# Performance work log

Hardware: AMD Instinct MI355X
Metric: run time of the kernel (lower is better)

The kernel has to match this reference:

```python
import jax, jax.numpy as jnp
import numpy as np

NUM_FREQS = 6

def posenc(x, num_freqs):
    freqs = (2.0 ** jnp.arange(num_freqs)).astype(x.dtype)  # [F]
    ang = x[..., None] * freqs                               # [N, D, F]
    enc = jnp.concatenate([jnp.sin(ang), jnp.cos(ang)], axis=-1)  # [N, D, 2F]
    return enc.reshape(x.shape[0], -1)

def setup_inputs() -> dict:
    key = jax.random.key(0)
    k1, k2, k3 = jax.random.split(key, 3)
    N, D, C = 200000, 6, 256
    E = D * 2 * NUM_FREQS  # 72
    X = jax.random.normal(k1, (N, D), dtype=jnp.float32)
    linear_mappings = jax.random.normal(k2, (3 * C, E), dtype=jnp.float32) * 0.05
    centroids = jax.random.normal(k3, (C, 3), dtype=jnp.float32)
    return {"X": X, "linear_mappings": linear_mappings, "centroids": centroids}

def reference(X, linear_mappings, centroids):
    N = X.shape[0]
    encoded_X = posenc(X, NUM_FREQS)                         # [N, E]
    rgb_clusters = encoded_X @ linear_mappings.T             # [N, 3C]
    rgb_clusters = rgb_clusters.reshape(N, -1, 3)            # [N, C, 3]
    # scores = centroids @ X[:, :3].T  -> softmax over clusters per point
    scores = X[:, :3] @ centroids.T                          # [N, C] (== scores.T in torch code)
    attention_weights = jax.nn.softmax(scores, axis=-1)      # [N, C]
    # torch does diagonal(attn @ rgb_clusters).T == per-row contraction:
    rgb = jnp.einsum('nc,ncd->nd', attention_weights, rgb_clusters)  # [N, 3]
    return rgb
```

## Files before the change

### kernel.cpp

```cpp
#include <hip/hip_runtime.h>
#include <math.h>


#define NCLUST   256
#define M_BLK    128
#define THREADS  256
#define NTILES   15
#define BG_BYTES (NTILES * 8 * 64 * 16)
#define ENC_STRIDE 168

typedef __attribute__((ext_vector_type(8))) short bfrag_t;
typedef __attribute__((ext_vector_type(4))) float cfrag_t;

static __device__ __forceinline__ unsigned int f2bf_u(float f) {
    unsigned int u = __float_as_uint(f);
    u += 0x7fffu + ((u >> 16) & 1u);
    return u >> 16;
}
static __device__ __forceinline__ unsigned int f2bf2(float lo, float hi) {
    return f2bf_u(lo) | (f2bf_u(hi) << 16);
}
static __device__ __forceinline__ float bf2f(unsigned short s) {
    return __uint_as_float(((unsigned int)s) << 16);
}
static __device__ __forceinline__ void glds16(const void* g, void* l) {
    __builtin_amdgcn_global_load_lds(
        (const __attribute__((address_space(1))) unsigned int*)g,
        (__attribute__((address_space(3))) unsigned int*)l, 16, 0, 0);
}

__global__ void prep_kernel(const float* __restrict__ W, uint4* __restrict__ Bg) {
    const int u = blockIdx.x * 256 + threadIdx.x;
    if (u >= NTILES * 8 * 64) return;
    const int lane = u & 63, ks = (u >> 6) & 7, tile = u >> 9;
    const int ln = lane & 15, q = lane >> 4;
    const int jp = tile * 16 + ln;
    const int d  = jp / 80;
    const int e  = jp - d * 80;
    const int c0 = ks * 32 + q * 8;
    unsigned int w[4] = {0u, 0u, 0u, 0u};
    if (e < 72) {
#pragma unroll
        for (int i = 0; i < 4; ++i) {
            float f0 = W[((c0 + 2 * i)     * 3 + d) * 72 + e];
            float f1 = W[((c0 + 2 * i + 1) * 3 + d) * 72 + e];
            w[i] = f2bf2(f0, f1);
        }
    }
    Bg[u] = make_uint4(w[0], w[1], w[2], w[3]);
}

__global__ __launch_bounds__(THREADS, 2) void rgb_attn_mfma(
    const float* __restrict__ X,
    const float* __restrict__ cent,
    const void* __restrict__ Bg,
    float* __restrict__ out, int N)
{
    __shared__ __align__(16) unsigned char encL[M_BLK * ENC_STRIDE];
    __shared__ __align__(16) unsigned char ABbuf[16384];
    __shared__ float denomL[M_BLK * 2];

    const int tid  = threadIdx.x;
    const int lane = tid & 63;
    const int wv   = tid >> 6;
    const int q    = lane >> 4;
    const int ln   = lane & 15;

    const int pt  = tid & 127;
    const int h   = tid >> 7;
    const int gpt = blockIdx.x * M_BLK + pt;
    const int gp  = (gpt < N) ? gpt : (N - 1);

    float x[6];
#pragma unroll
    for (int k = 0; k < 6; ++k) x[k] = X[gp * 6 + k];

    {
        const int row = tid >> 1, half = tid & 1;
        *(uint2*)(encL + row * ENC_STRIDE + 144 + half * 8) = make_uint2(0u, 0u);
    }
#pragma unroll
    for (int k = 0; k < 3; ++k) {
        const int dd = 3 * h + k;
        const float xv = x[dd];
        float s0,c0,s1,c1,s2,c2,s3,c3,s4,c4,s5,c5;
        __sincosf(xv *  1.0f, &s0, &c0);
        __sincosf(xv *  2.0f, &s1, &c1);
        __sincosf(xv *  4.0f, &s2, &c2);
        __sincosf(xv *  8.0f, &s3, &c3);
        __sincosf(xv * 16.0f, &s4, &c4);
        __sincosf(xv * 32.0f, &s5, &c5);
        unsigned char* rp = encL + pt * ENC_STRIDE + dd * 24;
        *(uint2*)(rp +  0) = make_uint2(f2bf2(s0, s1), f2bf2(s2, s3));
        *(uint2*)(rp +  8) = make_uint2(f2bf2(s4, s5), f2bf2(c0, c1));
        *(uint2*)(rp + 16) = make_uint2(f2bf2(c2, c3), f2bf2(c4, c5));
    }

    bfrag_t afrag[2][8];
    float dpart = 0.0f;
    uint4* AB4 = (uint4*)ABbuf;
#pragma unroll
    for (int p = 0; p < 4; ++p) {
        unsigned int pk[16];
#pragma unroll
        for (int i = 0; i < 16; ++i) {
            const int c0 = p * 64 + h * 32 + 2 * i;
            float sa = fmaf(x[0], cent[c0*3+0], fmaf(x[1], cent[c0*3+1], x[2]*cent[c0*3+2]));
            float sb = fmaf(x[0], cent[c0*3+3], fmaf(x[1], cent[c0*3+4], x[2]*cent[c0*3+5]));
            float ea = __expf(sa), eb_ = __expf(sb);
            dpart += ea + eb_;
            pk[i] = f2bf2(ea, eb_);
        }
        const int bu = ((pt >> 4) * 2 + h) * 64 + (pt & 15);
#pragma unroll
        for (int qq = 0; qq < 4; ++qq)
            AB4[bu + qq * 16] = make_uint4(pk[qq*4+0], pk[qq*4+1], pk[qq*4+2], pk[qq*4+3]);
        if (p == 3) denomL[pt * 2 + h] = dpart;
        __syncthreads();
#pragma unroll
        for (int mt = 0; mt < 2; ++mt)
#pragma unroll
            for (int kw = 0; kw < 2; ++kw)
                afrag[mt][2*p+kw] = *(const bfrag_t*)
                    (ABbuf + (((2*wv+mt)*2 + kw)*64 + lane)*16);
        __syncthreads();
    }

    float part[3][2][4] = {};

#define CONSUME_TILE(T, CT) { \
        cfrag_t a0 = {0.f,0.f,0.f,0.f}, a1 = {0.f,0.f,0.f,0.f}; \
        _Pragma("unroll") \
        for (int ks = 0; ks < 8; ++ks) { \
            const bfrag_t b = *(const bfrag_t*) \
                (ABbuf + (((CT)*8 + ks)*64 + lane)*16); \
            a0 = __builtin_amdgcn_mfma_f32_16x16x32_bf16(afrag[0][ks], b, a0, 0,0,0); \
            a1 = __builtin_amdgcn_mfma_f32_16x16x32_bf16(afrag[1][ks], b, a1, 0,0,0); \
        } \
        const int ebx = ((T) % 5) * 16 + ln; \
        _Pragma("unroll") \
        for (int mt = 0; mt < 2; ++mt) \
        _Pragma("unroll") \
        for (int r = 0; r < 4; ++r) { \
            const int pm = (2*wv + mt)*16 + q*4 + r; \
            const unsigned short us = *(const unsigned short*)(encL + pm*ENC_STRIDE + ebx*2); \
            part[(T)/5][mt][r] = fmaf((mt ? a1[r] : a0[r]), bf2f(us), part[(T)/5][mt][r]); \
        } \
    }

#define STAGE_CHUNK(CC, UNITS) { \
        __syncthreads(); \
        _Pragma("unroll") \
        for (int i = 0; i < 256; i += 64) { \
            if (i < (UNITS) / 4) { \
                const int u = wv * ((UNITS) / 4) + i + lane; \
                glds16((const char*)Bg + ((CC)*1024 + u)*16, (char*)ABbuf + u*16); \
            } } \
        __syncthreads(); \
    }

#define DO_CHUNK_FULL(CC) { \
        STAGE_CHUNK(CC, 1024); \
        CONSUME_TILE(2*(CC), 0); \
        CONSUME_TILE(2*(CC)+1, 1); \
    }

    DO_CHUNK_FULL(0) DO_CHUNK_FULL(1) DO_CHUNK_FULL(2) DO_CHUNK_FULL(3)
    DO_CHUNK_FULL(4) DO_CHUNK_FULL(5) DO_CHUNK_FULL(6)
    { STAGE_CHUNK(7, 512); CONSUME_TILE(14, 0); }

#pragma unroll
    for (int mask = 1; mask <= 8; mask <<= 1)
#pragma unroll
        for (int d = 0; d < 3; ++d)
#pragma unroll
            for (int mt = 0; mt < 2; ++mt)
#pragma unroll
                for (int r = 0; r < 4; ++r)
                    part[d][mt][r] += __shfl_xor(part[d][mt][r], mask, 64);

    if (ln == 0) {
#pragma unroll
        for (int mt = 0; mt < 2; ++mt)
#pragma unroll
            for (int r = 0; r < 4; ++r) {
                const int pm = (2*wv + mt)*16 + q*4 + r;
                const int g  = blockIdx.x * M_BLK + pm;
                if (g < N) {
                    const float inv = 1.0f / (denomL[pm*2] + denomL[pm*2+1]);
                    out[g*3+0] = part[0][mt][r] * inv;
                    out[g*3+1] = part[1][mt][r] * inv;
                    out[g*3+2] = part[2][mt][r] * inv;
                }
            }
    }
}

__global__ __launch_bounds__(256) void rgb_attn_fallback(
    const float* __restrict__ X, const float* __restrict__ W,
    const float* __restrict__ cent, float* __restrict__ out, int N)
{
    const int n = blockIdx.x * 256 + threadIdx.x;
    const bool valid = (n < N);
    float x[6];
#pragma unroll
    for (int k = 0; k < 6; ++k) x[k] = valid ? X[n * 6 + k] : 0.0f;
    float enc[72];
#pragma unroll
    for (int d = 0; d < 6; ++d)
#pragma unroll
        for (int f = 0; f < 6; ++f) {
            float s, c;
            __sincosf(x[d] * (float)(1 << f), &s, &c);
            enc[d*12+f] = s; enc[d*12+6+f] = c;
        }
    float acc0 = 0, acc1 = 0, acc2 = 0, denom = 0;
#pragma unroll 1
    for (int c = 0; c < NCLUST; ++c) {
        float s = fmaf(x[0], cent[c*3], fmaf(x[1], cent[c*3+1], x[2]*cent[c*3+2]));
        float ew = __expf(s);
        const float* w = W + c * 216;
        float d0 = 0, d1 = 0, d2 = 0;
#pragma unroll
        for (int e = 0; e < 72; ++e) {
            float ee = enc[e];
            d0 = fmaf(ee, w[e], d0);
            d1 = fmaf(ee, w[72 + e], d1);
            d2 = fmaf(ee, w[144 + e], d2);
        }
        denom += ew;
        acc0 = fmaf(ew, d0, acc0); acc1 = fmaf(ew, d1, acc1); acc2 = fmaf(ew, d2, acc2);
    }
    if (valid) {
        float inv = 1.0f / denom;
        out[n*3+0] = acc0*inv; out[n*3+1] = acc1*inv; out[n*3+2] = acc2*inv;
    }
}

extern "C" void kernel_launch(void* const* d_in, const int* in_sizes, int n_in,
                              void* d_out, int out_size, void* d_ws, size_t ws_size,
                              hipStream_t stream)
{
    const float* X    = (const float*)d_in[0];
    const float* W    = (const float*)d_in[1];
    const float* cent = (const float*)d_in[2];
    float* out = (float*)d_out;
    const int N = in_sizes[0] / 6;

    if (ws_size >= (size_t)BG_BYTES) {
        uint4* Bg = (uint4*)d_ws;
        prep_kernel<<<(NTILES * 8 * 64 + 255) / 256, 256, 0, stream>>>(W, Bg);
        const int blocks = (N + M_BLK - 1) / M_BLK;
        rgb_attn_mfma<<<blocks, THREADS, 0, stream>>>(X, cent, (const void*)Bg, out, N);
    } else {
        rgb_attn_fallback<<<(N + 255) / 256, 256, 0, stream>>>(X, W, cent, out, N);
    }
}
```

Before: 129.8 us.

## Stream B fragments from global into registers with prefetch; transpose encoding LDS layout

Replaces the LDS staging of the weight fragments (global_load_lds plus two barriers per chunk) with direct per-wave global loads into registers, double-buffered so the next tile's fragments load while the current tile's MFMAs run. The positional-encoding buffer is transposed so each lane reads four consecutive point values with one 8-byte LDS load instead of four 2-byte loads. This removes block-wide synchronization in the main loop, but each wave now fetches the full weight set from L2 separately. The rolled tile loop indexes the partial-sum array with a runtime index, which risks scratch spills or extra selects, and the second fragment buffer adds register pressure.

```diff
diff --git a/kernel.cpp b/kernel.cpp
--- a/kernel.cpp
+++ b/kernel.cpp
@@ -7,7 +7,7 @@
 #define THREADS  256
 #define NTILES   15
 #define BG_BYTES (NTILES * 8 * 64 * 16)
-#define ENC_STRIDE 168
+#define ENCT_STRIDE 272
 
 typedef __attribute__((ext_vector_type(8))) short bfrag_t;
 typedef __attribute__((ext_vector_type(4))) float cfrag_t;
@@ -20,13 +20,11 @@
 static __device__ __forceinline__ unsigned int f2bf2(float lo, float hi) {
     return f2bf_u(lo) | (f2bf_u(hi) << 16);
 }
-static __device__ __forceinline__ float bf2f(unsigned short s) {
-    return __uint_as_float(((unsigned int)s) << 16);
-}
-static __device__ __forceinline__ void glds16(const void* g, void* l) {
-    __builtin_amdgcn_global_load_lds(
-        (const __attribute__((address_space(1))) unsigned int*)g,
-        (__attribute__((address_space(3))) unsigned int*)l, 16, 0, 0);
+static __device__ __forceinline__ float bf2f_lo(unsigned int u) {
+    return __uint_as_float(u << 16);
+}
+static __device__ __forceinline__ float bf2f_hi(unsigned int u) {
+    return __uint_as_float(u & 0xffff0000u);
 }
 
 __global__ void prep_kernel(const float* __restrict__ W, uint4* __restrict__ Bg) {
@@ -56,8 +54,8 @@
     const void* __restrict__ Bg,
     float* __restrict__ out, int N)
 {
-    __shared__ __align__(16) unsigned char encL[M_BLK * ENC_STRIDE];
-    __shared__ __align__(16) unsigned char ABbuf[16384];
+    __shared__ __align__(16) unsigned char encT[80 * ENCT_STRIDE];
+    __shared__ __align__(16) unsigned char ABuf[16384];
     __shared__ float denomL[M_BLK * 2];
 
     const int tid  = threadIdx.x;
@@ -76,8 +74,8 @@
     for (int k = 0; k < 6; ++k) x[k] = X[gp * 6 + k];
 
     {
-        const int row = tid >> 1, half = tid & 1;
-        *(uint2*)(encL + row * ENC_STRIDE + 144 + half * 8) = make_uint2(0u, 0u);
+        const int col = 72 + (tid >> 5), rowg = tid & 31;
+        *(uint2*)(encT + col * ENCT_STRIDE + rowg * 8) = make_uint2(0u, 0u);
     }
 #pragma unroll
     for (int k = 0; k < 3; ++k) {
@@ -90,15 +88,24 @@
         __sincosf(xv *  8.0f, &s3, &c3);
         __sincosf(xv * 16.0f, &s4, &c4);
         __sincosf(xv * 32.0f, &s5, &c5);
-        unsigned char* rp = encL + pt * ENC_STRIDE + dd * 24;
-        *(uint2*)(rp +  0) = make_uint2(f2bf2(s0, s1), f2bf2(s2, s3));
-        *(uint2*)(rp +  8) = make_uint2(f2bf2(s4, s5), f2bf2(c0, c1));
-        *(uint2*)(rp + 16) = make_uint2(f2bf2(c2, c3), f2bf2(c4, c5));
+        unsigned char* base = encT + pt * 2 + (dd * 12) * ENCT_STRIDE;
+        *(unsigned short*)(base + 0 * ENCT_STRIDE)  = (unsigned short)f2bf_u(s0);
+        *(unsigned short*)(base + 1 * ENCT_STRIDE)  = (unsigned short)f2bf_u(s1);
+        *(unsigned short*)(base + 2 * ENCT_STRIDE)  = (unsigned short)f2bf_u(s2);
+        *(unsigned short*)(base + 3 * ENCT_STRIDE)  = (unsigned short)f2bf_u(s3);
+        *(unsigned short*)(base + 4 * ENCT_STRIDE)  = (unsigned short)f2bf_u(s4);
+        *(unsigned short*)(base + 5 * ENCT_STRIDE)  = (unsigned short)f2bf_u(s5);
+        *(unsigned short*)(base + 6 * ENCT_STRIDE)  = (unsigned short)f2bf_u(c0);
+        *(unsigned short*)(base + 7 * ENCT_STRIDE)  = (unsigned short)f2bf_u(c1);
+        *(unsigned short*)(base + 8 * ENCT_STRIDE)  = (unsigned short)f2bf_u(c2);
+        *(unsigned short*)(base + 9 * ENCT_STRIDE)  = (unsigned short)f2bf_u(c3);
+        *(unsigned short*)(base + 10 * ENCT_STRIDE) = (unsigned short)f2bf_u(c4);
+        *(unsigned short*)(base + 11 * ENCT_STRIDE) = (unsigned short)f2bf_u(c5);
     }
 
     bfrag_t afrag[2][8];
     float dpart = 0.0f;
-    uint4* AB4 = (uint4*)ABbuf;
+    uint4* AB4 = (uint4*)ABuf;
 #pragma unroll
     for (int p = 0; p < 4; ++p) {
         unsigned int pk[16];
@@ -122,52 +129,49 @@
 #pragma unroll
             for (int kw = 0; kw < 2; ++kw)
                 afrag[mt][2*p+kw] = *(const bfrag_t*)
-                    (ABbuf + (((2*wv+mt)*2 + kw)*64 + lane)*16);
+                    (ABuf + (((2*wv+mt)*2 + kw)*64 + lane)*16);
         __syncthreads();
     }
 
     float part[3][2][4] = {};
-
-#define CONSUME_TILE(T, CT) { \
-        cfrag_t a0 = {0.f,0.f,0.f,0.f}, a1 = {0.f,0.f,0.f,0.f}; \
-        _Pragma("unroll") \
-        for (int ks = 0; ks < 8; ++ks) { \
-            const bfrag_t b = *(const bfrag_t*) \
-                (ABbuf + (((CT)*8 + ks)*64 + lane)*16); \
-            a0 = __builtin_amdgcn_mfma_f32_16x16x32_bf16(afrag[0][ks], b, a0, 0,0,0); \
-            a1 = __builtin_amdgcn_mfma_f32_16x16x32_bf16(afrag[1][ks], b, a1, 0,0,0); \
-        } \
-        const int ebx = ((T) % 5) * 16 + ln; \
-        _Pragma("unroll") \
-        for (int mt = 0; mt < 2; ++mt) \
-        _Pragma("unroll") \
-        for (int r = 0; r < 4; ++r) { \
-            const int pm = (2*wv + mt)*16 + q*4 + r; \
-            const unsigned short us = *(const unsigned short*)(encL + pm*ENC_STRIDE + ebx*2); \
-            part[(T)/5][mt][r] = fmaf((mt ? a1[r] : a0[r]), bf2f(us), part[(T)/5][mt][r]); \
-        } \
-    }
-
-#define STAGE_CHUNK(CC, UNITS) { \
-        __syncthreads(); \
-        _Pragma("unroll") \
-        for (int i = 0; i < 256; i += 64) { \
-            if (i < (UNITS) / 4) { \
-                const int u = wv * ((UNITS) / 4) + i + lane; \
-                glds16((const char*)Bg + ((CC)*1024 + u)*16, (char*)ABbuf + u*16); \
-            } } \
-        __syncthreads(); \
-    }
-
-#define DO_CHUNK_FULL(CC) { \
-        STAGE_CHUNK(CC, 1024); \
-        CONSUME_TILE(2*(CC), 0); \
-        CONSUME_TILE(2*(CC)+1, 1); \
-    }
-
-    DO_CHUNK_FULL(0) DO_CHUNK_FULL(1) DO_CHUNK_FULL(2) DO_CHUNK_FULL(3)
-    DO_CHUNK_FULL(4) DO_CHUNK_FULL(5) DO_CHUNK_FULL(6)
-    { STAGE_CHUNK(7, 512); CONSUME_TILE(14, 0); }
+    const char* bgp = (const char*)Bg + lane * 16;
+
+    bfrag_t bc[8], bn[8];
+#pragma unroll
+    for (int ks = 0; ks < 8; ++ks)
+        bc[ks] = *(const bfrag_t*)(bgp + ks * 1024);
+
+#pragma unroll 1
+    for (int t = 0; t < NTILES; ++t) {
+        const char* nxt = bgp + (t + 1) * 8192;
+        if (t < NTILES - 1) {
+#pragma unroll
+            for (int ks = 0; ks < 8; ++ks)
+                bn[ks] = *(const bfrag_t*)(nxt + ks * 1024);
+        }
+        cfrag_t a0 = {0.f,0.f,0.f,0.f}, a1 = {0.f,0.f,0.f,0.f};
+#pragma unroll
+        for (int ks = 0; ks < 8; ++ks) {
+            a0 = __builtin_amdgcn_mfma_f32_16x16x32_bf16(afrag[0][ks], bc[ks], a0, 0,0,0);
+            a1 = __builtin_amdgcn_mfma_f32_16x16x32_bf16(afrag[1][ks], bc[ks], a1, 0,0,0);
+        }
+        const int tm5 = (t >= 10) ? (t - 10) : ((t >= 5) ? (t - 5) : t);
+        const int dblk = (t >= 10) ? 2 : ((t >= 5) ? 1 : 0);
+        const int ebx = tm5 * 16 + ln;
+#pragma unroll
+        for (int mt = 0; mt < 2; ++mt) {
+            const int row0 = (2*wv + mt)*16 + q*4;
+            const uint2 ev = *(const uint2*)(encT + ebx * ENCT_STRIDE + row0 * 2);
+            const float e0 = bf2f_lo(ev.x), e1 = bf2f_hi(ev.x);
+            const float e2 = bf2f_lo(ev.y), e3 = bf2f_hi(ev.y);
+            part[dblk][mt][0] = fmaf((mt ? a1[0] : a0[0]), e0, part[dblk][mt][0]);
+            part[dblk][mt][1] = fmaf((mt ? a1[1] : a0[1]), e1, part[dblk][mt][1]);
+            part[dblk][mt][2] = fmaf((mt ? a1[2] : a0[2]), e2, part[dblk][mt][2]);
+            part[dblk][mt][3] = fmaf((mt ? a1[3] : a0[3]), e3, part[dblk][mt][3]);
+        }
+#pragma unroll
+        for (int ks = 0; ks < 8; ++ks) bc[ks] = bn[ks];
+    }
 
 #pragma unroll
     for (int mask = 1; mask <= 8; mask <<= 1)
```

After: 149.8 us. 15.4% more time.

## Double-buffer per-tile B staging to overlap global loads with MFMA

Applied to the files above, without the earlier changes.

Replaces the two-tile chunk staging, which used a sync-load-sync pattern, with a per-tile double-buffered pipeline. The next tile's weights are prefetched via direct global-to-LDS loads into the alternate buffer while the current tile is multiplied, and there is one barrier per tile. The launch-bounds occupancy hint also rises from 2 to 3 blocks per CU, which may squeeze registers given the large afrag and part arrays held per thread. Loads are now issued 8KB at a time, and there is a risk of relying on barrier semantics for completion of the async LDS loads.

```diff
diff --git a/kernel.cpp b/kernel.cpp
--- a/kernel.cpp
+++ b/kernel.cpp
@@ -50,14 +50,14 @@
     Bg[u] = make_uint4(w[0], w[1], w[2], w[3]);
 }
 
-__global__ __launch_bounds__(THREADS, 2) void rgb_attn_mfma(
+__global__ __launch_bounds__(THREADS, 3) void rgb_attn_mfma(
     const float* __restrict__ X,
     const float* __restrict__ cent,
     const void* __restrict__ Bg,
     float* __restrict__ out, int N)
 {
     __shared__ __align__(16) unsigned char encL[M_BLK * ENC_STRIDE];
-    __shared__ __align__(16) unsigned char ABbuf[16384];
+    __shared__ __align__(16) unsigned char Bbuf[2][8192];
     __shared__ float denomL[M_BLK * 2];
 
     const int tid  = threadIdx.x;
@@ -98,7 +98,7 @@
 
     bfrag_t afrag[2][8];
     float dpart = 0.0f;
-    uint4* AB4 = (uint4*)ABbuf;
+    uint4* AB4 = (uint4*)&Bbuf[0][0];
 #pragma unroll
     for (int p = 0; p < 4; ++p) {
         unsigned int pk[16];
@@ -122,52 +122,51 @@
 #pragma unroll
             for (int kw = 0; kw < 2; ++kw)
                 afrag[mt][2*p+kw] = *(const bfrag_t*)
-                    (ABbuf + (((2*wv+mt)*2 + kw)*64 + lane)*16);
+                    (&Bbuf[0][0] + (((2*wv+mt)*2 + kw)*64 + lane)*16);
         __syncthreads();
     }
 
     float part[3][2][4] = {};
 
-#define CONSUME_TILE(T, CT) { \
-        cfrag_t a0 = {0.f,0.f,0.f,0.f}, a1 = {0.f,0.f,0.f,0.f}; \
-        _Pragma("unroll") \
-        for (int ks = 0; ks < 8; ++ks) { \
-            const bfrag_t b = *(const bfrag_t*) \
-                (ABbuf + (((CT)*8 + ks)*64 + lane)*16); \
-            a0 = __builtin_amdgcn_mfma_f32_16x16x32_bf16(afrag[0][ks], b, a0, 0,0,0); \
-            a1 = __builtin_amdgcn_mfma_f32_16x16x32_bf16(afrag[1][ks], b, a1, 0,0,0); \
-        } \
-        const int ebx = ((T) % 5) * 16 + ln; \
-        _Pragma("unroll") \
-        for (int mt = 0; mt < 2; ++mt) \
-        _Pragma("unroll") \
-        for (int r = 0; r < 4; ++r) { \
-            const int pm = (2*wv + mt)*16 + q*4 + r; \
-            const unsigned short us = *(const unsigned short*)(encL + pm*ENC_STRIDE + ebx*2); \
-            part[(T)/5][mt][r] = fmaf((mt ? a1[r] : a0[r]), bf2f(us), part[(T)/5][mt][r]); \
-        } \
-    }
-
-#define STAGE_CHUNK(CC, UNITS) { \
-        __syncthreads(); \
-        _Pragma("unroll") \
-        for (int i = 0; i < 256; i += 64) { \
-            if (i < (UNITS) / 4) { \
-                const int u = wv * ((UNITS) / 4) + i + lane; \
-                glds16((const char*)Bg + ((CC)*1024 + u)*16, (char*)ABbuf + u*16); \
-            } } \
-        __syncthreads(); \
-    }
-
-#define DO_CHUNK_FULL(CC) { \
-        STAGE_CHUNK(CC, 1024); \
-        CONSUME_TILE(2*(CC), 0); \
-        CONSUME_TILE(2*(CC)+1, 1); \
-    }
-
-    DO_CHUNK_FULL(0) DO_CHUNK_FULL(1) DO_CHUNK_FULL(2) DO_CHUNK_FULL(3)
-    DO_CHUNK_FULL(4) DO_CHUNK_FULL(5) DO_CHUNK_FULL(6)
-    { STAGE_CHUNK(7, 512); CONSUME_TILE(14, 0); }
+#pragma unroll
+    for (int i = 0; i < 2; ++i) {
+        const int u = wv * 128 + i * 64 + lane;
+        glds16((const char*)Bg + u * 16, &Bbuf[0][0] + u * 16);
+    }
+    __syncthreads();
+
+#pragma unroll
+    for (int t = 0; t < NTILES; ++t) {
+        if (t < NTILES - 1) {
+#pragma unroll
+            for (int i = 0; i < 2; ++i) {
+                const int u = wv * 128 + i * 64 + lane;
+                glds16((const char*)Bg + (t + 1) * 8192 + u * 16,
+                       &Bbuf[(t + 1) & 1][0] + u * 16);
+            }
+        }
+        cfrag_t a0 = {0.f,0.f,0.f,0.f}, a1 = {0.f,0.f,0.f,0.f};
+#pragma unroll
+        for (int ks = 0; ks < 8; ++ks) {
+            const bfrag_t b = *(const bfrag_t*)
+                (&Bbuf[t & 1][0] + (ks * 64 + lane) * 16);
+            a0 = __builtin_amdgcn_mfma_f32_16x16x32_bf16(afrag[0][ks], b, a0, 0,0,0);
+            a1 = __builtin_amdgcn_mfma_f32_16x16x32_bf16(afrag[1][ks], b, a1, 0,0,0);
+        }
+        const int dblk = t / 5;
+        const int ebx  = (t % 5) * 16 + ln;
+#pragma unroll
+        for (int mt = 0; mt < 2; ++mt)
+#pragma unroll
+            for (int r = 0; r < 4; ++r) {
+                const int pm = (2*wv + mt)*16 + q*4 + r;
+                const unsigned short us =
+                    *(const unsigned short*)(encL + pm*ENC_STRIDE + ebx*2);
+                part[dblk][mt][r] = fmaf((mt ? a1[r] : a0[r]), bf2f(us),
+                                         part[dblk][mt][r]);
+            }
+        __syncthreads();
+    }
 
 #pragma unroll
     for (int mask = 1; mask <= 8; mask <<= 1)
```

Result: slower. 176.7 us (+36.2%).
